# Kernel optimization log

Hardware: AMD Instinct MI355X
Metric: run time of the kernel (lower is better)

The kernel has to match this reference:

```python
import jax, jax.numpy as jnp
import numpy as np

TOPK = 10
NUM_CLASSES = 80
ALPHA = 0.5
BETA = 6.0
EPS = 1e-9


def setup_inputs() -> dict:
    key = jax.random.key(0)
    ks = jax.random.split(key, 7)
    bs, A, n, C = 16, 8400, 64, NUM_CLASSES
    pd_scores = jax.random.uniform(ks[0], (bs, A, C), jnp.float32)
    # valid xyxy boxes inside a 640x640 image
    pxy = jax.random.uniform(ks[1], (bs, A, 2), jnp.float32) * 576.0
    pwh = jax.random.uniform(ks[2], (bs, A, 2), jnp.float32) * 64.0 + 8.0
    pd_bboxes = jnp.concatenate([pxy, pxy + pwh], axis=-1)
    gxy = jax.random.uniform(ks[3], (bs, n, 2), jnp.float32) * 576.0
    gwh = jax.random.uniform(ks[4], (bs, n, 2), jnp.float32) * 64.0 + 8.0
    gt_bboxes = jnp.concatenate([gxy, gxy + gwh], axis=-1)
    anc_points = jax.random.uniform(ks[5], (A, 2), jnp.float32) * 640.0
    gt_labels = jax.random.randint(ks[6], (bs, n, 1), 0, C, dtype=jnp.int32)
    return {"pd_scores": pd_scores, "pd_bboxes": pd_bboxes,
            "anc_points": anc_points, "gt_labels": gt_labels,
            "gt_bboxes": gt_bboxes}


def _iou(gt_bboxes, pd_bboxes, eps=EPS):
    # gt_bboxes: (bs, n, 4), pd_bboxes: (bs, A, 4) -> (bs, n, A)
    b1 = gt_bboxes[:, :, None, :]
    b2 = pd_bboxes[:, None, :, :]
    lt = jnp.maximum(b1[..., :2], b2[..., :2])
    rb = jnp.minimum(b1[..., 2:], b2[..., 2:])
    overlap = jnp.clip(rb - lt, 0).prod(-1)
    area1 = jnp.clip(b1[..., 2:] - b1[..., :2], 0).prod(-1)
    area2 = jnp.clip(b2[..., 2:] - b2[..., :2], 0).prod(-1)
    return overlap / (area1 + area2 - overlap + eps)


def _assign(pd_scores, pd_bboxes, anc_points, gt_labels, gt_bboxes):
    bs, A, C = pd_scores.shape
    n = gt_bboxes.shape[1]
    dt = pd_scores.dtype
    labels = gt_labels[..., 0]                       # (bs, n)
    # ---- box metrics: gather class score per gt (bs, n, A) ----
    bi = jnp.arange(bs)[:, None]                     # (bs, 1)
    bbox_scores = pd_scores[bi, :, labels]           # (bs, n, A)
    overlaps = _iou(gt_bboxes, pd_bboxes)            # (bs, n, A)
    align_metric = bbox_scores ** ALPHA * overlaps ** BETA
    # ---- anchor-center-in-gt mask ----
    lt = gt_bboxes[..., None, :2]                    # (bs, n, 1, 2)
    rb = gt_bboxes[..., None, 2:]
    anc = anc_points[None, None]                     # (1, 1, A, 2)
    deltas_min = jnp.minimum((anc - lt).min(-1), (rb - anc).min(-1))
    mask_in_gts = (deltas_min > EPS).astype(dt)      # (bs, n, A)
    # ---- top-k candidates per gt (scatter-add instead of huge one-hot) ----
    metrics = align_metric * mask_in_gts
    topk_vals, topk_idxs = jax.lax.top_k(metrics, TOPK)
    valid = topk_vals.max(-1, keepdims=True) > EPS
    topk_idxs = jnp.where(valid, topk_idxs, 0)
    bi3 = jnp.arange(bs)[:, None, None]
    ni3 = jnp.arange(n)[None, :, None]
    cnt = jnp.zeros((bs, n, A), dt).at[bi3, ni3, topk_idxs].add(1.0)
    is_in_topk = jnp.where(cnt > 1, jnp.zeros((), dt), cnt)
    mask_pos = is_in_topk * mask_in_gts
    # ---- resolve anchors assigned to multiple gts via highest IoU ----
    fg_mask = mask_pos.sum(-2)                       # (bs, A)
    mask_multi = fg_mask[:, None, :] > 1             # (bs, 1->n, A)
    is_max = jax.nn.one_hot(overlaps.argmax(1), n, axis=1, dtype=dt)  # (bs, n, A)
    mask_pos = jnp.where(mask_multi, is_max, mask_pos)
    fg_mask = mask_pos.sum(-2)
    target_gt_idx = mask_pos.argmax(-2)              # (bs, A)
    # ---- gather targets ----
    flat_idx = target_gt_idx + jnp.arange(bs)[:, None] * n
    target_labels = jnp.maximum(labels.reshape(-1)[flat_idx], 0)
    target_bboxes = gt_bboxes.reshape(-1, 4)[flat_idx]
    target_scores = jax.nn.one_hot(target_labels, C, dtype=dt)
    target_scores = jnp.where(fg_mask[..., None] > 0, target_scores,
                              jnp.zeros((), dt))
    # ---- normalize scores by task-aligned metric ----
    align_metric = align_metric * mask_pos
    pos_align = align_metric.max(-1, keepdims=True)
    pos_over = (overlaps * mask_pos).max(-1, keepdims=True)
    norm = (align_metric * pos_over / (pos_align + EPS)).max(-2)[..., None]
    target_scores = target_scores * norm
    return target_labels, target_bboxes, target_scores, fg_mask > 0


def reference(pd_scores, pd_bboxes, anc_points, gt_labels, gt_bboxes):
    return _assign(pd_scores, pd_bboxes, anc_points, gt_labels, gt_bboxes)
```

## Files before the change

kernel.cpp:

```cpp
#include <hip/hip_runtime.h>

#define TOPK 10
#define EPSF 1e-9f
#define CHUNKS 4

typedef unsigned long long u64;
typedef unsigned int u32;

__global__ __launch_bounds__(256) void k_init(uint4* __restrict__ p, int n16) {
    int i = blockIdx.x * 256 + threadIdx.x;
    if (i < n16) p[i] = make_uint4(0, 0, 0, 0);
}

__global__ __launch_bounds__(256) void k_chunk(
    const float* __restrict__ pd_scores, const float* __restrict__ pd_bboxes,
    const float* __restrict__ anc, const int* __restrict__ gt_labels,
    const float* __restrict__ gt_bboxes,
    float* __restrict__ overlaps, u64* __restrict__ part,
    int A, int n, int C)
{
    __shared__ u64 sk[256 * 11];

    const int row = blockIdx.y;
    const int b   = row / n;
    const int tid = threadIdx.x;
    const int CS  = (A + CHUNKS - 1) / CHUNKS;
    const int a0  = blockIdx.x * CS;
    const int a1  = min(A, a0 + CS);

    const float4 g = *(const float4*)(gt_bboxes + (size_t)row * 4);
    const int    c = gt_labels[row];
    const float* ps = pd_scores + (size_t)b * A * C + c;
    const float4* pb = (const float4*)(pd_bboxes + (size_t)b * A * 4);
    const float2* an2 = (const float2*)anc;
    const size_t rowbase = (size_t)row * A;
    const float ga = fmaxf(g.z - g.x, 0.f) * fmaxf(g.w - g.y, 0.f);

    u64 tk[TOPK];
    #pragma unroll
    for (int k = 0; k < TOPK; ++k) tk[k] = 0;

    for (int a = a0 + tid; a < a1; a += 256) {
        float4 p = pb[a];
        float ow = fmaxf(fminf(g.z, p.z) - fmaxf(g.x, p.x), 0.f) *
                   fmaxf(fminf(g.w, p.w) - fmaxf(g.y, p.y), 0.f);
        float pa = fmaxf(p.z - p.x, 0.f) * fmaxf(p.w - p.y, 0.f);
        float iou = ow / (ga + pa - ow + EPSF);
        overlaps[rowbase + a] = iou;

        float2 ap = an2[a];
        float dmin = fminf(fminf(ap.x - g.x, ap.y - g.y),
                           fminf(g.z - ap.x, g.w - ap.y));
        float met = 0.f;
        if (dmin > EPSF) met = sqrtf(ps[(size_t)a * C]) * powf(iou, 6.0f);

        u64 key = ((u64)__float_as_uint(met) << 32) | (u32)(0x7fffffff - a);
        if (key > tk[TOPK-1]) {
            tk[TOPK-1] = key;
            #pragma unroll
            for (int k = TOPK-1; k > 0; --k)
                if (tk[k] > tk[k-1]) { u64 t = tk[k]; tk[k] = tk[k-1]; tk[k-1] = t; }
        }
    }

    #pragma unroll
    for (int k = 0; k < TOPK; ++k) sk[tid * 11 + k] = tk[k];

    for (int s = 128; s > 0; s >>= 1) {
        __syncthreads();
        if (tid < s) {
            const int bA = tid * 11, bB = (tid + s) * 11;
            int pa_ = 0, pb_ = 0;
            u64 out[TOPK];
            #pragma unroll
            for (int k = 0; k < TOPK; ++k) {
                u64 va = sk[bA + pa_], vb = sk[bB + pb_];
                bool ta = va > vb;
                out[k] = ta ? va : vb;
                pa_ += ta; pb_ += !ta;
            }
            #pragma unroll
            for (int k = 0; k < TOPK; ++k) sk[bA + k] = out[k];
        }
    }
    __syncthreads();

    if (tid < TOPK)
        part[((size_t)row * CHUNKS + blockIdx.x) * TOPK + tid] = sk[tid];
}

__global__ __launch_bounds__(256) void k_merge(
    const float* __restrict__ anc, const float* __restrict__ gt_bboxes,
    const u64* __restrict__ part, u64* __restrict__ mask64,
    int A, int n, int R)
{
    int row = blockIdx.x * 256 + threadIdx.x;
    if (row >= R) return;
    int b = row / n;
    int j = row - b * n;
    const u64* l = part + (size_t)row * CHUNKS * TOPK;
    const float4 g = *(const float4*)(gt_bboxes + (size_t)row * 4);
    const float2* an2 = (const float2*)anc;

    int p0 = 0, p1 = 0, p2 = 0, p3 = 0;
    for (int k = 0; k < TOPK; ++k) {
        u64 v0 = (p0 < TOPK) ? l[p0]            : 0;
        u64 v1 = (p1 < TOPK) ? l[TOPK + p1]     : 0;
        u64 v2 = (p2 < TOPK) ? l[2 * TOPK + p2] : 0;
        u64 v3 = (p3 < TOPK) ? l[3 * TOPK + p3] : 0;
        u64 bv = v0; int best = 0;
        if (v1 > bv) { bv = v1; best = 1; }
        if (v2 > bv) { bv = v2; best = 2; }
        if (v3 > bv) { bv = v3; best = 3; }
        p0 += (best == 0); p1 += (best == 1);
        p2 += (best == 2); p3 += (best == 3);

        if (k == 0) {
            float m0 = __uint_as_float((u32)(bv >> 32));
            if (!(m0 > EPSF)) break;
        }
        int a = 0x7fffffff - (int)(u32)(bv & 0xffffffffu);
        float2 ap = an2[a];
        float dmin = fminf(fminf(ap.x - g.x, ap.y - g.y),
                           fminf(g.z - ap.x, g.w - ap.y));
        if (dmin > EPSF)
            atomicOr(&mask64[(size_t)b * A + a], 1ull << j);
    }
}

__global__ __launch_bounds__(256) void k_col(
    const float* __restrict__ pd_scores,
    const int* __restrict__ gt_labels, const float* __restrict__ gt_bboxes,
    const float* __restrict__ overlaps, u64* __restrict__ mask64,
    float* __restrict__ out_labels, float* __restrict__ out_bboxes,
    float* __restrict__ out_fg,
    float* __restrict__ pos_align, float* __restrict__ pos_over,
    int A, int n, int C)
{
    __shared__ float4 sg[64];
    __shared__ int    sl[64];
    const int b = blockIdx.y;
    const int a = blockIdx.x * 256 + threadIdx.x;
    if (threadIdx.x < n) {
        sg[threadIdx.x] = ((const float4*)gt_bboxes)[b * n + threadIdx.x];
        sl[threadIdx.x] = gt_labels[b * n + threadIdx.x];
    }
    __syncthreads();
    if (a >= A) return;

    const size_t midx = (size_t)b * A + a;
    u64 m = mask64[midx];
    int pc = __popcll(m);
    int jt = 0;
    if (pc > 1) {
        const float* col = overlaps + (size_t)b * n * A + a;
        float bv = col[0]; int bj = 0;
        for (int jj = 1; jj < n; ++jj) {
            float v = col[(size_t)jj * A];
            if (v > bv) { bv = v; bj = jj; }
        }
        jt = bj; mask64[midx] = 1ull << bj; pc = 1;
    } else if (pc == 1) {
        jt = __ffsll(m) - 1;
    }

    int lab = sl[jt];
    out_labels[midx] = (float)(lab < 0 ? 0 : lab);
    ((float4*)out_bboxes)[midx] = sg[jt];
    out_fg[midx] = pc ? 1.f : 0.f;

    if (pc) {
        int rowj = b * n + jt;
        float iou = overlaps[(size_t)rowj * A + a];
        float s = pd_scores[((size_t)b * A + a) * C + lab];
        float al = sqrtf(s) * powf(iou, 6.0f);
        atomicMax((int*)&pos_align[rowj], __float_as_int(al));
        atomicMax((int*)&pos_over[rowj],  __float_as_int(iou));
    }
}

__global__ __launch_bounds__(256) void k_norm(
    const float* __restrict__ pd_scores, const int* __restrict__ gt_labels,
    const float* __restrict__ overlaps, const u64* __restrict__ mask64,
    const float* __restrict__ pos_align, const float* __restrict__ pos_over,
    float* __restrict__ normv, int A, int n, int C, int total)
{
    int idx = blockIdx.x * 256 + threadIdx.x;
    if (idx >= total) return;
    int b = idx / A;
    int a = idx - b * A;
    u64 m = mask64[idx];
    float nm = 0.f;
    if (m) {
        int jj = __ffsll(m) - 1;
        int rowj = b * n + jj;
        float iou = overlaps[(size_t)rowj * A + a];
        float s = pd_scores[(size_t)idx * C + gt_labels[rowj]];
        float al = sqrtf(s) * powf(iou, 6.0f);
        nm = al * pos_over[rowj] / (pos_align[rowj] + EPSF);
    }
    normv[idx] = nm;
}

__global__ __launch_bounds__(256) void k_scores(
    const float* __restrict__ out_labels, const float* __restrict__ out_fg,
    const float* __restrict__ normv, float4* __restrict__ out_scores,
    int C4, int quads)
{
    int idx = blockIdx.x * 256 + threadIdx.x;
    if (idx >= quads) return;
    int ba = idx / C4;
    int q  = idx - ba * C4;
    float4 v = make_float4(0.f, 0.f, 0.f, 0.f);
    if (out_fg[ba] > 0.f) {
        int r = (int)out_labels[ba] - q * 4;
        float nv = normv[ba];
        v.x = (r == 0) ? nv : 0.f;
        v.y = (r == 1) ? nv : 0.f;
        v.z = (r == 2) ? nv : 0.f;
        v.w = (r == 3) ? nv : 0.f;
    }
    out_scores[idx] = v;
}

extern "C" void kernel_launch(void* const* d_in, const int* in_sizes, int n_in,
                              void* d_out, int out_size, void* d_ws, size_t ws_size,
                              hipStream_t stream)
{
    const float* pd_scores = (const float*)d_in[0];
    const float* pd_bboxes = (const float*)d_in[1];
    const float* anc       = (const float*)d_in[2];
    const int*   gt_labels = (const int*)d_in[3];
    const float* gt_bboxes = (const float*)d_in[4];

    const int C  = 80;
    const int A  = in_sizes[2] / 2;
    const int bs = in_sizes[0] / (A * C);
    const int n  = in_sizes[3] / bs;
    const int R  = bs * n;
    const int BA = bs * A;

    size_t off = 0;
    u64*   mask64    = (u64*)((char*)d_ws + off);   off += (size_t)BA * 8;
    float* pos_align = (float*)((char*)d_ws + off); off += (size_t)R * 4;
    float* pos_over  = (float*)((char*)d_ws + off); off += (size_t)R * 4;
    size_t zero_bytes = off;
    float* overlaps  = (float*)((char*)d_ws + off); off += (size_t)R * A * 4;
    float* normv     = (float*)((char*)d_ws + off); off += (size_t)BA * 4;
    u64*   part      = (u64*)((char*)d_ws + off);   off += (size_t)R * CHUNKS * TOPK * 8;

    float* out_labels = (float*)d_out;
    float* out_bboxes = out_labels + (size_t)BA;
    float* out_scores = out_bboxes + (size_t)BA * 4;
    float* out_fg     = out_scores + (size_t)BA * C;

    int n16 = (int)(zero_bytes / 16);
    k_init<<<(n16 + 255) / 256, 256, 0, stream>>>((uint4*)d_ws, n16);

    k_chunk<<<dim3(CHUNKS, R), 256, 0, stream>>>(
        pd_scores, pd_bboxes, anc, gt_labels, gt_bboxes, overlaps, part, A, n, C);

    k_merge<<<(R + 255) / 256, 256, 0, stream>>>(
        anc, gt_bboxes, part, mask64, A, n, R);

    k_col<<<dim3((A + 255) / 256, bs), 256, 0, stream>>>(
        pd_scores, gt_labels, gt_bboxes, overlaps, mask64,
        out_labels, out_bboxes, out_fg, pos_align, pos_over, A, n, C);

    k_norm<<<(BA + 255) / 256, 256, 0, stream>>>(
        pd_scores, gt_labels, overlaps, mask64, pos_align, pos_over,
        normv, A, n, C, BA);

    int quads = BA * (C / 4);
    k_scores<<<(quads + 255) / 256, 256, 0, stream>>>(
        out_labels, out_fg, normv, (float4*)out_scores, C / 4, quads);
}
```

Measured before the change: 172.5 us.

## Use one wavefront per row-chunk with shuffle top-k reduction instead of LDS tree

```diff
diff --git a/kernel.cpp b/kernel.cpp
--- a/kernel.cpp
+++ b/kernel.cpp
@@ -2,7 +2,7 @@
 
 #define TOPK 10
 #define EPSF 1e-9f
-#define CHUNKS 4
+#define CHUNKS 8
 
 typedef unsigned long long u64;
 typedef unsigned int u32;
@@ -19,14 +19,14 @@
     float* __restrict__ overlaps, u64* __restrict__ part,
     int A, int n, int C)
 {
-    __shared__ u64 sk[256 * 11];
-
-    const int row = blockIdx.y;
-    const int b   = row / n;
-    const int tid = threadIdx.x;
-    const int CS  = (A + CHUNKS - 1) / CHUNKS;
-    const int a0  = blockIdx.x * CS;
-    const int a1  = min(A, a0 + CS);
+    const int gw   = blockIdx.x * 4 + (threadIdx.x >> 6);
+    const int lane = threadIdx.x & 63;
+    const int row  = gw >> 3;
+    const int ch   = gw & (CHUNKS - 1);
+    const int b    = row / n;
+    const int CS   = (A + CHUNKS - 1) / CHUNKS;
+    const int a0   = ch * CS;
+    const int a1   = min(A, a0 + CS);
 
     const float4 g = *(const float4*)(gt_bboxes + (size_t)row * 4);
     const int    c = gt_labels[row];
@@ -40,7 +40,7 @@
     #pragma unroll
     for (int k = 0; k < TOPK; ++k) tk[k] = 0;
 
-    for (int a = a0 + tid; a < a1; a += 256) {
+    for (int a = a0 + lane; a < a1; a += 64) {
         float4 p = pb[a];
         float ow = fmaxf(fminf(g.z, p.z) - fmaxf(g.x, p.x), 0.f) *
                    fmaxf(fminf(g.w, p.w) - fmaxf(g.y, p.y), 0.f);
@@ -63,38 +63,32 @@
         }
     }
 
+    u64 mine = 0;
     #pragma unroll
-    for (int k = 0; k < TOPK; ++k) sk[tid * 11 + k] = tk[k];
-
-    for (int s = 128; s > 0; s >>= 1) {
-        __syncthreads();
-        if (tid < s) {
-            const int bA = tid * 11, bB = (tid + s) * 11;
-            int pa_ = 0, pb_ = 0;
-            u64 out[TOPK];
+    for (int r = 0; r < TOPK; ++r) {
+        u64 m = tk[0];
+        #pragma unroll
+        for (int s = 1; s < 64; s <<= 1) {
+            u64 o = __shfl_xor(m, s, 64);
+            m = (o > m) ? o : m;
+        }
+        if (lane == r) mine = m;
+        if (tk[0] == m) {
             #pragma unroll
-            for (int k = 0; k < TOPK; ++k) {
-                u64 va = sk[bA + pa_], vb = sk[bB + pb_];
-                bool ta = va > vb;
-                out[k] = ta ? va : vb;
-                pa_ += ta; pb_ += !ta;
-            }
-            #pragma unroll
-            for (int k = 0; k < TOPK; ++k) sk[bA + k] = out[k];
-        }
-    }
-    __syncthreads();
-
-    if (tid < TOPK)
-        part[((size_t)row * CHUNKS + blockIdx.x) * TOPK + tid] = sk[tid];
-}
-
-__global__ __launch_bounds__(256) void k_merge(
+            for (int k = 0; k < TOPK - 1; ++k) tk[k] = tk[k + 1];
+            tk[TOPK-1] = 0;
+        }
+    }
+    if (lane < TOPK)
+        part[((size_t)row * CHUNKS + ch) * TOPK + lane] = mine;
+}
+
+__global__ __launch_bounds__(64) void k_merge(
     const float* __restrict__ anc, const float* __restrict__ gt_bboxes,
     const u64* __restrict__ part, u64* __restrict__ mask64,
     int A, int n, int R)
 {
-    int row = blockIdx.x * 256 + threadIdx.x;
+    int row = blockIdx.x * 64 + threadIdx.x;
     if (row >= R) return;
     int b = row / n;
     int j = row - b * n;
@@ -102,18 +96,26 @@
     const float4 g = *(const float4*)(gt_bboxes + (size_t)row * 4);
     const float2* an2 = (const float2*)anc;
 
-    int p0 = 0, p1 = 0, p2 = 0, p3 = 0;
+    int p0 = 0, p1 = 0, p2 = 0, p3 = 0, p4 = 0, p5 = 0, p6 = 0, p7 = 0;
     for (int k = 0; k < TOPK; ++k) {
-        u64 v0 = (p0 < TOPK) ? l[p0]            : 0;
-        u64 v1 = (p1 < TOPK) ? l[TOPK + p1]     : 0;
-        u64 v2 = (p2 < TOPK) ? l[2 * TOPK + p2] : 0;
-        u64 v3 = (p3 < TOPK) ? l[3 * TOPK + p3] : 0;
+        u64 v0 = (p0 < TOPK) ? l[0*TOPK + p0] : 0;
+        u64 v1 = (p1 < TOPK) ? l[1*TOPK + p1] : 0;
+        u64 v2 = (p2 < TOPK) ? l[2*TOPK + p2] : 0;
+        u64 v3 = (p3 < TOPK) ? l[3*TOPK + p3] : 0;
+        u64 v4 = (p4 < TOPK) ? l[4*TOPK + p4] : 0;
+        u64 v5 = (p5 < TOPK) ? l[5*TOPK + p5] : 0;
+        u64 v6 = (p6 < TOPK) ? l[6*TOPK + p6] : 0;
+        u64 v7 = (p7 < TOPK) ? l[7*TOPK + p7] : 0;
         u64 bv = v0; int best = 0;
         if (v1 > bv) { bv = v1; best = 1; }
         if (v2 > bv) { bv = v2; best = 2; }
         if (v3 > bv) { bv = v3; best = 3; }
-        p0 += (best == 0); p1 += (best == 1);
-        p2 += (best == 2); p3 += (best == 3);
+        if (v4 > bv) { bv = v4; best = 4; }
+        if (v5 > bv) { bv = v5; best = 5; }
+        if (v6 > bv) { bv = v6; best = 6; }
+        if (v7 > bv) { bv = v7; best = 7; }
+        p0 += (best == 0); p1 += (best == 1); p2 += (best == 2); p3 += (best == 3);
+        p4 += (best == 4); p5 += (best == 5); p6 += (best == 6); p7 += (best == 7);
 
         if (k == 0) {
             float m0 = __uint_as_float((u32)(bv >> 32));
@@ -257,10 +259,10 @@
     int n16 = (int)(zero_bytes / 16);
     k_init<<<(n16 + 255) / 256, 256, 0, stream>>>((uint4*)d_ws, n16);
 
-    k_chunk<<<dim3(CHUNKS, R), 256, 0, stream>>>(
+    k_chunk<<<R * CHUNKS / 4, 256, 0, stream>>>(
         pd_scores, pd_bboxes, anc, gt_labels, gt_bboxes, overlaps, part, A, n, C);
 
-    k_merge<<<(R + 255) / 256, 256, 0, stream>>>(
+    k_merge<<<(R + 63) / 64, 64, 0, stream>>>(
         anc, gt_bboxes, part, mask64, A, n, R);
 
     k_col<<<dim3((A + 255) / 256, bs), 256, 0, stream>>>(
```

After: 169.0 us. -2.0%, faster.
